# Optimization experiments

Hardware: AMD Instinct MI355X
Metric: run time of the kernel (lower is better)

## Reference

```python
import jax, jax.numpy as jnp
import numpy as np

N = 2048          # number of glyph samples
SRC = 64          # raw alpha map size
PAD = 32          # zero padding on each side -> 128x128 source
HIN = SRC + 2 * PAD   # 128
WIN = SRC + 2 * PAD   # 128
TH = SRC * 2      # target_h = 2 * targetsize (=64) -> 128
TW = SRC * 2


def setup_inputs() -> dict:
    key = jax.random.key(0)
    k1, k2, k3 = jax.random.split(key, 3)
    return {
        "affine_outs": jax.random.normal(k1, (N, 6), jnp.float32),
        "fill_alpha": jax.random.uniform(k2, (N, SRC, SRC), jnp.float32),
        "stroke_alpha": jax.random.uniform(k3, (N, SRC, SRC), jnp.float32),
        # all target sizes fixed to 64 (-> 128x128 output) for static shapes
        "targetsize": jnp.full((1, N, 2), SRC, jnp.int32),
    }


def _theta(affine_outs):
    # matches torch.split(affine_outs, 1, 1) ordering: 00,11,01,10,02,12
    a00 = jax.nn.sigmoid(affine_outs[:, 0]) * 2.0
    a11 = jax.nn.sigmoid(affine_outs[:, 1]) * 2.0
    a01 = jnp.tanh(affine_outs[:, 2]) * 2.0
    a10 = jnp.tanh(affine_outs[:, 3]) * 2.0
    a02 = jnp.tanh(affine_outs[:, 4])
    a12 = jnp.tanh(affine_outs[:, 5])
    row1 = jnp.stack([a00, a01, a02], axis=-1)  # [N,3]
    row2 = jnp.stack([a10, a11, a12], axis=-1)  # [N,3]
    return jnp.stack([row1, row2], axis=1)      # [N,2,3]


def _affine_grid(theta):
    # F.affine_grid align_corners=False base grid for (TH, TW)
    xs = (jnp.arange(TW, dtype=jnp.float32) + 0.5) * (2.0 / TW) - 1.0  # [TW]
    ys = (jnp.arange(TH, dtype=jnp.float32) + 0.5) * (2.0 / TH) - 1.0  # [TH]
    X = xs[None, :]  # broadcast to [TH,TW]
    Y = ys[:, None]
    t = theta[:, :, :, None, None]  # [N,2,3,1,1]
    gx = t[:, 0, 0] * X + t[:, 0, 1] * Y + t[:, 0, 2]  # [N,TH,TW]
    gy = t[:, 1, 0] * X + t[:, 1, 1] * Y + t[:, 1, 2]
    return gx, gy


def _bilinear_zeros(img, ix, iy):
    # grid_sample(mode='bilinear', padding_mode='zeros', align_corners=False)
    n = img.shape[0]
    b = jnp.arange(n)[:, None, None]
    x0 = jnp.floor(ix)
    y0 = jnp.floor(iy)
    wx = ix - x0
    wy = iy - y0

    def fetch(xf, yf):
        xi = jnp.clip(xf, 0, WIN - 1).astype(jnp.int32)
        yi = jnp.clip(yf, 0, HIN - 1).astype(jnp.int32)
        v = img[b, yi, xi]
        valid = (xf >= 0) & (xf <= WIN - 1) & (yf >= 0) & (yf <= HIN - 1)
        return jnp.where(valid, v, 0.0)

    return (fetch(x0, y0) * (1 - wx) * (1 - wy)
            + fetch(x0 + 1, y0) * wx * (1 - wy)
            + fetch(x0, y0 + 1) * (1 - wx) * wy
            + fetch(x0 + 1, y0 + 1) * wx * wy)


def reference(affine_outs, fill_alpha, stroke_alpha, targetsize):
    theta = _theta(affine_outs)
    gx, gy = _affine_grid(theta)
    # normalized -> pixel coords (align_corners=False)
    ix = ((gx + 1.0) * WIN - 1.0) * 0.5
    iy = ((gy + 1.0) * HIN - 1.0) * 0.5
    pad = ((0, 0), (PAD, PAD), (PAD, PAD))
    fill_p = jnp.pad(fill_alpha, pad)
    stroke_p = jnp.pad(stroke_alpha, pad)
    fill_out = _bilinear_zeros(fill_p, ix, iy)      # [N,TH,TW]
    stroke_out = _bilinear_zeros(stroke_p, ix, iy)  # [N,TH,TW]
    return fill_out, stroke_out
```

## Files before the change

kernel.cpp:

```cpp
#include <hip/hip_runtime.h>

#define N_IMG 2048
#define SRC   64
#define PADW  32
#define TH    128
#define TW    128

#define LPAD  66
#define LSZ   (LPAD + SRC * SRC + 66)

__global__ __launch_bounds__(256) void affine_sample_kernel(
    const float* __restrict__ affine,
    const float* __restrict__ fill,
    const float* __restrict__ stroke,
    float* __restrict__ out)
{
    __shared__ float2 sFS[LSZ];

    const int n = blockIdx.x;
    const float* __restrict__ fptr = fill   + (size_t)n * SRC * SRC;
    const float* __restrict__ sptr = stroke + (size_t)n * SRC * SRC;

    if (threadIdx.x < LPAD) {
        sFS[threadIdx.x] = make_float2(0.f, 0.f);
        sFS[LPAD + SRC * SRC + threadIdx.x] = make_float2(0.f, 0.f);
    }

    for (int i = threadIdx.x; i < SRC * SRC / 4; i += 256) {
        const float4 f = reinterpret_cast<const float4*>(fptr)[i];
        const float4 s = reinterpret_cast<const float4*>(sptr)[i];
        float2* dst = &sFS[LPAD + 4 * i];
        dst[0] = make_float2(f.x, s.x);
        dst[1] = make_float2(f.y, s.y);
        dst[2] = make_float2(f.z, s.z);
        dst[3] = make_float2(f.w, s.w);
    }

    const float t0 = affine[n * 6 + 0];
    const float t1 = affine[n * 6 + 1];
    const float t2 = affine[n * 6 + 2];
    const float t3 = affine[n * 6 + 3];
    const float t4 = affine[n * 6 + 4];
    const float t5 = affine[n * 6 + 5];
    const float a00 = 2.0f / (1.0f + __expf(-t0));
    const float a11 = 2.0f / (1.0f + __expf(-t1));
    const float a01 = 2.0f * tanhf(t2);
    const float a10 = 2.0f * tanhf(t3);
    const float a02 = tanhf(t4);
    const float a12 = tanhf(t5);

    __syncthreads();

    float* __restrict__ outF = out + (size_t)n * TH * TW;
    float* __restrict__ outS = out + (size_t)N_IMG * TH * TW + (size_t)n * TH * TW;

    for (int q = threadIdx.x; q < TH * TW / 4; q += 256) {
        const int py  = q >> 5;
        const int pxb = (q & 31) << 2;
        const float Y  = ((float)py + 0.5f) * (2.0f / TH) - 1.0f;
        const float Cx = 64.0f * (a01 * Y + a02 - a00) + 31.5f;
        const float Cy = 64.0f * (a11 * Y + a12 - a10) + 31.5f;

        float rf[4], rs[4];

        #pragma unroll
        for (int j = 0; j < 4; ++j) {
            const float fx  = (float)(pxb + j) + 0.5f;
            const float isx = fmaf(a00, fx, Cx);
            const float isy = fmaf(a10, fx, Cy);

            const float x0f = floorf(isx);
            const float y0f = floorf(isy);
            const float wx  = isx - x0f;
            const float wy  = isy - y0f;
            const int   x0  = (int)x0f;
            const int   y0  = (int)y0f;

            const float wxa = ((unsigned)x0       < (unsigned)SRC) ? (1.0f - wx) : 0.0f;
            const float wxb = ((unsigned)(x0 + 1) < (unsigned)SRC) ? wx          : 0.0f;
            const float wya = ((unsigned)y0       < (unsigned)SRC) ? (1.0f - wy) : 0.0f;
            const float wyb = ((unsigned)(y0 + 1) < (unsigned)SRC) ? wy          : 0.0f;

            const int xc = min(max(x0, -1), SRC - 1);
            const int yc = min(max(y0, -1), SRC - 1);
            const int base = LPAD + yc * SRC + xc;

            const float2 v00 = sFS[base];
            const float2 v10 = sFS[base + 1];
            const float2 v01 = sFS[base + SRC];
            const float2 v11 = sFS[base + SRC + 1];

            const float w00 = wxa * wya;
            const float w10 = wxb * wya;
            const float w01 = wxa * wyb;
            const float w11 = wxb * wyb;

            rf[j] = w00 * v00.x + w10 * v10.x + w01 * v01.x + w11 * v11.x;
            rs[j] = w00 * v00.y + w10 * v10.y + w01 * v01.y + w11 * v11.y;
        }

        reinterpret_cast<float4*>(outF)[q] = make_float4(rf[0], rf[1], rf[2], rf[3]);
        reinterpret_cast<float4*>(outS)[q] = make_float4(rs[0], rs[1], rs[2], rs[3]);
    }
}

extern "C" void kernel_launch(void* const* d_in, const int* in_sizes, int n_in,
                              void* d_out, int out_size, void* d_ws, size_t ws_size,
                              hipStream_t stream) {
    const float* affine = (const float*)d_in[0];
    const float* fill   = (const float*)d_in[1];
    const float* stroke = (const float*)d_in[2];
    float* out = (float*)d_out;

    affine_sample_kernel<<<dim3(N_IMG), dim3(256), 0, stream>>>(affine, fill, stroke, out);
}
```

Baseline: 356.8 us.

## Use 2-pixel zero-bordered planar LDS tiles and lane-strided output mapping

Replaces the interleaved float2 shared buffer with two separate 68x68 fill and stroke tiles that carry a 2-pixel zero border. Clamping indices into that border removes the per-tap bounds checks on the bilinear weights. Output pixels are now assigned lane-contiguously: each lane writes scalar floats at stride 32 instead of float4 vectors, which changes the LDS access pattern and may reduce bank conflicts. The cost is more scalar LDS reads and stores, narrower global stores, and a more complex zero-fill of the border.

```diff
diff --git a/kernel.cpp b/kernel.cpp
--- a/kernel.cpp
+++ b/kernel.cpp
@@ -2,12 +2,12 @@
 
 #define N_IMG 2048
 #define SRC   64
-#define PADW  32
 #define TH    128
 #define TW    128
+#define LW    68
+#define LN    (LW * LW)
 
-#define LPAD  66
-#define LSZ   (LPAD + SRC * SRC + 66)
+typedef float v2f __attribute__((ext_vector_type(2)));
 
 __global__ __launch_bounds__(256) void affine_sample_kernel(
     const float* __restrict__ affine,
@@ -15,25 +15,33 @@
     const float* __restrict__ stroke,
     float* __restrict__ out)
 {
-    __shared__ float2 sFS[LSZ];
+    __shared__ float sF[LN];
+    __shared__ float sS[LN];
 
-    const int n = blockIdx.x;
+    const int n   = blockIdx.x;
+    const int tid = threadIdx.x;
+
+    for (int i = tid; i < 136; i += 256) {
+        const int r = i / LW, c = i % LW;
+        sF[r * LW + c] = 0.f;  sF[(67 - r) * LW + c] = 0.f;
+        sS[r * LW + c] = 0.f;  sS[(67 - r) * LW + c] = 0.f;
+    }
+    for (int i = tid; i < 128; i += 256) {
+        const int r = 2 + (i >> 1), c = i & 1;
+        sF[r * LW + c] = 0.f;  sF[r * LW + 67 - c] = 0.f;
+        sS[r * LW + c] = 0.f;  sS[r * LW + 67 - c] = 0.f;
+    }
+
     const float* __restrict__ fptr = fill   + (size_t)n * SRC * SRC;
     const float* __restrict__ sptr = stroke + (size_t)n * SRC * SRC;
-
-    if (threadIdx.x < LPAD) {
-        sFS[threadIdx.x] = make_float2(0.f, 0.f);
-        sFS[LPAD + SRC * SRC + threadIdx.x] = make_float2(0.f, 0.f);
-    }
-
-    for (int i = threadIdx.x; i < SRC * SRC / 4; i += 256) {
+    for (int i = tid; i < SRC * SRC / 4; i += 256) {
         const float4 f = reinterpret_cast<const float4*>(fptr)[i];
         const float4 s = reinterpret_cast<const float4*>(sptr)[i];
-        float2* dst = &sFS[LPAD + 4 * i];
-        dst[0] = make_float2(f.x, s.x);
-        dst[1] = make_float2(f.y, s.y);
-        dst[2] = make_float2(f.z, s.z);
-        dst[3] = make_float2(f.w, s.w);
+        const int y  = i >> 4;
+        const int x4 = (i & 15) << 2;
+        const int d  = (y + 2) * LW + x4 + 2;
+        sF[d] = f.x; sF[d + 1] = f.y; sF[d + 2] = f.z; sF[d + 3] = f.w;
+        sS[d] = s.x; sS[d + 1] = s.y; sS[d + 2] = s.z; sS[d + 3] = s.w;
     }
 
     const float t0 = affine[n * 6 + 0];
@@ -54,18 +62,20 @@
     float* __restrict__ outF = out + (size_t)n * TH * TW;
     float* __restrict__ outS = out + (size_t)N_IMG * TH * TW + (size_t)n * TH * TW;
 
-    for (int q = threadIdx.x; q < TH * TW / 4; q += 256) {
-        const int py  = q >> 5;
-        const int pxb = (q & 31) << 2;
+    const int lane = tid & 31;
+    const int rsub = tid >> 5;
+
+    for (int it = 0; it < 16; ++it) {
+        const int py = it * 8 + rsub;
         const float Y  = ((float)py + 0.5f) * (2.0f / TH) - 1.0f;
         const float Cx = 64.0f * (a01 * Y + a02 - a00) + 31.5f;
         const float Cy = 64.0f * (a11 * Y + a12 - a10) + 31.5f;
-
-        float rf[4], rs[4];
+        float* __restrict__ oF = outF + py * TW + lane;
+        float* __restrict__ oS = outS + py * TW + lane;
 
         #pragma unroll
         for (int j = 0; j < 4; ++j) {
-            const float fx  = (float)(pxb + j) + 0.5f;
+            const float fx  = (float)(lane + 32 * j) + 0.5f;
             const float isx = fmaf(a00, fx, Cx);
             const float isy = fmaf(a10, fx, Cy);
 
@@ -73,34 +83,24 @@
             const float y0f = floorf(isy);
             const float wx  = isx - x0f;
             const float wy  = isy - y0f;
-            const int   x0  = (int)x0f;
-            const int   y0  = (int)y0f;
 
-            const float wxa = ((unsigned)x0       < (unsigned)SRC) ? (1.0f - wx) : 0.0f;
-            const float wxb = ((unsigned)(x0 + 1) < (unsigned)SRC) ? wx          : 0.0f;
-            const float wya = ((unsigned)y0       < (unsigned)SRC) ? (1.0f - wy) : 0.0f;
-            const float wyb = ((unsigned)(y0 + 1) < (unsigned)SRC) ? wy          : 0.0f;
+            const int xc = min(max((int)x0f, -2), 64);
+            const int yc = min(max((int)y0f, -2), 64);
+            const int idx = (yc + 2) * LW + (xc + 2);
 
-            const int xc = min(max(x0, -1), SRC - 1);
-            const int yc = min(max(y0, -1), SRC - 1);
-            const int base = LPAD + yc * SRC + xc;
+            v2f v00 = { sF[idx],          sS[idx]          };
+            v2f v10 = { sF[idx + 1],      sS[idx + 1]      };
+            v2f v01 = { sF[idx + LW],     sS[idx + LW]     };
+            v2f v11 = { sF[idx + LW + 1], sS[idx + LW + 1] };
 
-            const float2 v00 = sFS[base];
-            const float2 v10 = sFS[base + 1];
-            const float2 v01 = sFS[base + SRC];
-            const float2 v11 = sFS[base + SRC + 1];
+            const float wxa = 1.0f - wx;
+            const float wya = 1.0f - wy;
+            v2f r = (wxa * wya) * v00 + (wx * wya) * v10
+                  + (wxa * wy ) * v01 + (wx * wy ) * v11;
 
-            const float w00 = wxa * wya;
-            const float w10 = wxb * wya;
-            const float w01 = wxa * wyb;
-            const float w11 = wxb * wyb;
-
-            rf[j] = w00 * v00.x + w10 * v10.x + w01 * v01.x + w11 * v11.x;
-            rs[j] = w00 * v00.y + w10 * v10.y + w01 * v01.y + w11 * v11.y;
+            oF[32 * j] = r.x;
+            oS[32 * j] = r.y;
         }
-
-        reinterpret_cast<float4*>(outF)[q] = make_float4(rf[0], rf[1], rf[2], rf[3]);
-        reinterpret_cast<float4*>(outS)[q] = make_float4(rs[0], rs[1], rs[2], rs[3]);
     }
 }
 
```

Result: faster. 330.3 us (-7.4%).
